# Kernel optimization log

Hardware: AMD Instinct MI355X
Metric: run time of the kernel (lower is better)

Reference implementation:

```python
import jax, jax.numpy as jnp
import numpy as np

N = 20000      # nodes
E = 320000     # edges (before self loops)
IN = 128       # in_channels
HID = 256      # hidden_channels
HEADS = 8
C = HID // HEADS  # 32 per-head dim
L = 4          # num_gat_layers
BN_EPS = 1e-5
LN_EPS = 1e-5


def setup_inputs() -> dict:
    key = jax.random.key(0)
    ks = iter(jax.random.split(key, 64))
    def rn(shape, s=0.05):
        return jax.random.normal(next(ks), shape, jnp.float32) * s
    inp = {
        'x': jax.random.normal(next(ks), (N, IN), jnp.float32),
        'edge_index': jax.random.randint(next(ks), (2, E), 0, N),
        # FeatureMLP
        'mlp_w1': rn((IN, HID)), 'mlp_b1': jnp.zeros((HID,), jnp.float32),
        'bn1_g': jnp.ones((HID,), jnp.float32), 'bn1_b': jnp.zeros((HID,), jnp.float32),
        'mlp_w2': rn((HID, HID)), 'mlp_b2': jnp.zeros((HID,), jnp.float32),
        'bn2_g': jnp.ones((HID,), jnp.float32), 'bn2_b': jnp.zeros((HID,), jnp.float32),
        'mlp_w3': rn((HID, HID)), 'mlp_b3': jnp.zeros((HID,), jnp.float32),
        # stacked GATv2 layer params [L, ...]
        'gat_wl': rn((L, HID, HID)), 'gat_bl': jnp.zeros((L, HID), jnp.float32),
        'gat_wr': rn((L, HID, HID)), 'gat_br': jnp.zeros((L, HID), jnp.float32),
        'gat_att': rn((L, HEADS, C)), 'gat_bias': jnp.zeros((L, HID), jnp.float32),
        'ln_g': jnp.ones((L, HID), jnp.float32), 'ln_b': jnp.zeros((L, HID), jnp.float32),
        'head_w1': rn((2 * HID, HID)), 'head_b1': jnp.zeros((HID,), jnp.float32),
        'hbn1_g': jnp.ones((HID,), jnp.float32), 'hbn1_b': jnp.zeros((HID,), jnp.float32),
        'head_w2': rn((HID, HID // 2)), 'head_b2': jnp.zeros((HID // 2,), jnp.float32),
        'hbn2_g': jnp.ones((HID // 2,), jnp.float32), 'hbn2_b': jnp.zeros((HID // 2,), jnp.float32),
        'head_w3': rn((HID // 2, HID // 4)), 'head_b3': jnp.zeros((HID // 4,), jnp.float32),
        'head_w4': rn((HID // 4, 1)), 'head_b4': jnp.zeros((1,), jnp.float32),
    }
    return inp


def _lrelu01(v):
    return jax.nn.leaky_relu(v, 0.1)


def _bn_eval(v, g, b):
    # eval-mode BatchNorm1d with running_mean=0, running_var=1
    return v * (g / jnp.sqrt(1.0 + BN_EPS)) + b


def _layernorm(v, g, b):
    mu = jnp.mean(v, axis=-1, keepdims=True)
    var = jnp.mean((v - mu) ** 2, axis=-1, keepdims=True)
    return (v - mu) / jnp.sqrt(var + LN_EPS) * g + b


def _gatv2(x, src, dst, Wl, bl, Wr, br, att, bias):
    n = x.shape[0]
    xl = (x @ Wl + bl).reshape(n, HEADS, C)   # source transform
    xr = (x @ Wr + br).reshape(n, HEADS, C)   # target transform
    # per-edge attention logits (GATv2): a . LeakyReLU(x_l[src] + x_r[dst])
    e = jax.nn.leaky_relu(xl[src] + xr[dst], 0.2)          # [E, H, C]
    logits = jnp.einsum('ehc,hc->eh', e, att)               # [E, H]
    # segment softmax over destination nodes
    m = jax.ops.segment_max(logits, dst, num_segments=n)    # [N, H]
    a = jnp.exp(logits - m[dst])
    s = jax.ops.segment_sum(a, dst, num_segments=n)
    alpha = a / (s[dst] + 1e-16)                            # [E, H]
    out = jax.ops.segment_sum(xl[src] * alpha[:, :, None], dst, num_segments=n)
    return out.reshape(n, HID) + bias


def _forward(x, mlp_w1, mlp_b1, bn1_g, bn1_b, mlp_w2, mlp_b2, bn2_g, bn2_b,
             mlp_w3, mlp_b3, gat_wl, gat_bl, gat_wr, gat_br, gat_att, gat_bias,
             ln_g, ln_b, head_w1, head_b1, hbn1_g, hbn1_b, head_w2, head_b2,
             hbn2_g, hbn2_b, head_w3, head_b3, head_w4, head_b4, edge_index):
    n = x.shape[0]
    # FeatureMLP (eval: dropout off)
    h = _lrelu01(_bn_eval(x @ mlp_w1 + mlp_b1, bn1_g, bn1_b))
    h = _lrelu01(_bn_eval(h @ mlp_w2 + mlp_b2, bn2_g, bn2_b))
    x_mlp = h @ mlp_w3 + mlp_b3
    # add self loops
    loop = jnp.arange(n)
    src = jnp.concatenate([edge_index[0], loop])
    dst = jnp.concatenate([edge_index[1], loop])
    g = x_mlp
    for i in range(L):
        res = g
        o = _gatv2(g, src, dst, gat_wl[i], gat_bl[i], gat_wr[i], gat_br[i],
                   gat_att[i], gat_bias[i])
        o = _lrelu01(_layernorm(o, ln_g[i], ln_b[i]))
        g = o + res
    xc = jnp.concatenate([x_mlp, g], axis=1)                # [N, 2*HID]
    h = _lrelu01(_bn_eval(xc @ head_w1 + head_b1, hbn1_g, hbn1_b))
    h = _lrelu01(_bn_eval(h @ head_w2 + head_b2, hbn2_g, hbn2_b))
    h = _lrelu01(h @ head_w3 + head_b3)
    return h @ head_w4 + head_b4                            # [N, 1]


def reference(x, edge_index, mlp_w1, mlp_b1, bn1_g, bn1_b, mlp_w2, mlp_b2,
              bn2_g, bn2_b, mlp_w3, mlp_b3, gat_wl, gat_bl, gat_wr, gat_br,
              gat_att, gat_bias, ln_g, ln_b, head_w1, head_b1, hbn1_g, hbn1_b,
              head_w2, head_b2, hbn2_g, hbn2_b, head_w3, head_b3, head_w4, head_b4):
    return _forward(x, mlp_w1, mlp_b1, bn1_g, bn1_b, mlp_w2, mlp_b2, bn2_g,
                    bn2_b, mlp_w3, mlp_b3, gat_wl, gat_bl, gat_wr, gat_br,
                    gat_att, gat_bias, ln_g, ln_b, head_w1, head_b1, hbn1_g,
                    hbn1_b, head_w2, head_b2, hbn2_g, hbn2_b, head_w3, head_b3,
                    head_w4, head_b4, edge_index)
```

## Files before the change

kernel.cpp:

```cpp
#include <hip/hip_runtime.h>
#include <hip/hip_bf16.h>

#define N_NODES 20000
#define E_EDGES 320000
#define E_TOT   (E_EDGES + N_NODES)
#define IN_CH   128
#define HID     256
#define HEADS   8
#define CPH     32

enum { EP_BIAS = 0, EP_BN_LRELU = 1, EP_LRELU = 2 };

typedef _Float16 f16;
typedef f16  f16x2 __attribute__((ext_vector_type(2)));
typedef f16  f16x4 __attribute__((ext_vector_type(4)));
typedef f16  f16x8 __attribute__((ext_vector_type(8)));
typedef float f32x2 __attribute__((ext_vector_type(2)));
typedef float f32x4 __attribute__((ext_vector_type(4)));

__device__ __forceinline__ f16x2 h2max(f16x2 a, f16x2 b) {
#if __has_builtin(__builtin_elementwise_max)
    return __builtin_elementwise_max(a, b);
#else
    f16x2 r; r[0] = a[0] > b[0] ? a[0] : b[0]; r[1] = a[1] > b[1] ? a[1] : b[1]; return r;
#endif
}
__device__ __forceinline__ float hdot2(f16x2 a, f16x2 b, float c) {
#if __has_builtin(__builtin_amdgcn_fdot2)
    return __builtin_amdgcn_fdot2(a, b, c, false);
#else
    return c + (float)a[0] * (float)b[0] + (float)a[1] * (float)b[1];
#endif
}
__device__ __forceinline__ float fexp2(float x) {
#if __has_builtin(__builtin_amdgcn_exp2f)
    return __builtin_amdgcn_exp2f(x);
#else
    return exp2f(x);
#endif
}

__device__ __forceinline__ size_t frag_idx(int row, int col, int KB) {
    int kb = col >> 6, ks = (col >> 5) & 1, q = (col >> 3) & 3, e = col & 7;
    return ((((size_t)(row >> 4) * KB + kb) * 2 + ks) << 9) + (((q << 4) | (row & 15)) << 3) + e;
}

struct WDesc { const float* src; f16* dst; int K; int Nc; int NTOT; int ct0; };
struct WDescs { WDesc d[14]; };

#define WPREP_BLKS (14 * 512)
#define CVT_BLKS   ((N_NODES * IN_CH) / 256)
#define DEG_BLKS   ((E_EDGES + 255) / 256)
#define ZERO_BLKS  ((N_NODES + 255) / 256)
#define PREP_BLKS  (WPREP_BLKS + CVT_BLKS + DEG_BLKS + ZERO_BLKS)

__global__ __launch_bounds__(256)
void prep_kernel(WDescs ds, const float* __restrict__ x, f16* __restrict__ x16,
                 const int* __restrict__ dstE, int* __restrict__ cnt, int* __restrict__ cur)
{
    const int bx = blockIdx.x;
    const int tid = threadIdx.x;
    if (bx < WPREP_BLKS) {
        WDesc w = ds.d[bx >> 9];
        int i = ((bx & 511) << 8) + tid;
        if (i < w.K * w.Nc) {
            int NT_local = w.Nc >> 4;
            int e  = i & 7;
            int l  = (i >> 3) & 63;
            int r  = i >> 9;
            int ct = r % NT_local;
            int q  = r / NT_local;
            int ks = q & 1;
            int kb = q >> 1;
            int n  = ct * 16 + (l & 15);
            int k  = kb * 64 + ks * 32 + ((l >> 4) << 3) + e;
            size_t di = (((size_t)(kb * 2 + ks) * w.NTOT + w.ct0 + ct) << 9) + (l << 3) + e;
            w.dst[di] = (f16)w.src[(size_t)k * w.Nc + n];
        }
    } else if (bx < WPREP_BLKS + CVT_BLKS) {
        int i = (bx - WPREP_BLKS) * 256 + tid;
        if (i < N_NODES * IN_CH) {
            int row = i / IN_CH, col = i - row * IN_CH;
            x16[frag_idx(row, col, 2)] = (f16)x[i];
        }
    } else if (bx < WPREP_BLKS + CVT_BLKS + DEG_BLKS) {
        int e = (bx - WPREP_BLKS - CVT_BLKS) * 256 + tid;
        if (e < E_EDGES) atomicAdd(&cnt[dstE[e]], 1);
    } else {
        int i = (bx - WPREP_BLKS - CVT_BLKS - DEG_BLKS) * 256 + tid;
        if (i < N_NODES) cur[i] = 0;
    }
}

template<int NT, int NTOT, int WAVES, int RT, int DOT, int OUTF>
__global__ __launch_bounds__(WAVES * 64)
void gemm_kernel(const f16* __restrict__ A1, int KB1,
                 const f16* __restrict__ A2, int KB2,
                 const f16* __restrict__ Wf,
                 const float* __restrict__ biasA,
                 const float* __restrict__ biasB,
                 const float* __restrict__ bng,
                 const float* __restrict__ bnb,
                 f16* __restrict__ out16A,
                 f16* __restrict__ out16B,
                 f16* __restrict__ dup16,
                 float* __restrict__ out32,
                 const float* __restrict__ dotw,
                 const float* __restrict__ dotb,
                 float* __restrict__ outdot,
                 int NcA, int KBo, int mode)
{
    const int tid  = threadIdx.x;
    const int wave = tid >> 6;
    const int lane = tid & 63;
    const int quad = lane >> 4;
    const int rb0 = blockIdx.x * RT;
    const int KBt = KB1 + KB2;

    f32x4 acc[RT][NT];
#pragma unroll
    for (int t = 0; t < RT; ++t)
#pragma unroll
        for (int j = 0; j < NT; ++j) acc[t][j] = (f32x4){0.f, 0.f, 0.f, 0.f};

#pragma unroll 2
    for (int kb = 0; kb < KBt; ++kb) {
#pragma unroll
        for (int ks = 0; ks < 2; ++ks) {
            f16x8 a[RT];
#pragma unroll
            for (int t = 0; t < RT; ++t) {
                const f16* ap = (kb < KB1)
                    ? A1 + (((((size_t)(rb0 + t)) * KB1 + kb) * 2 + ks) << 9) + (lane << 3)
                    : A2 + (((((size_t)(rb0 + t)) * KB2 + (kb - KB1)) * 2 + ks) << 9) + (lane << 3);
                a[t] = *(const f16x8*)ap;
            }
            const f16* bp = Wf + (((size_t)(kb * 2 + ks) * NTOT + wave * NT) << 9) + (lane << 3);
#pragma unroll
            for (int ct = 0; ct < NT; ++ct) {
                f16x8 b = *(const f16x8*)(bp + ((size_t)ct << 9));
#pragma unroll
                for (int t = 0; t < RT; ++t)
                    acc[t][ct] = __builtin_amdgcn_mfma_f32_16x16x32_f16(a[t], b, acc[t][ct], 0, 0, 0);
            }
        }
    }

    const int c0 = lane & 15;
    const int NcB = NTOT * 16 - NcA;
#pragma unroll
    for (int t = 0; t < RT; ++t) {
        const int r0 = (rb0 + t) * 16 + (quad << 2);
#pragma unroll
        for (int ct = 0; ct < NT; ++ct) {
            int col = (wave * NT + ct) * 16 + c0;
            bool isB = col >= NcA;
            int colL = isB ? col - NcA : col;
            float bv = isB ? biasB[colL] : biasA[colL];
            float sc = 1.f, sh = 0.f;
            if (mode == EP_BN_LRELU) {
                sc = bng[col] * rsqrtf(1.f + 1e-5f);
                sh = bnb[col];
            }
#pragma unroll
            for (int reg = 0; reg < 4; ++reg) {
                int row = r0 + reg;
                float v = acc[t][ct][reg] + bv;
                if (mode == EP_BN_LRELU) { v = v * sc + sh; v = v > 0.f ? v : 0.1f * v; }
                else if (mode == EP_LRELU) { v = v > 0.f ? v : 0.1f * v; }
                if (OUTF) {
                    size_t idx = frag_idx(row, col, KBo);
                    out16A[idx] = (f16)v;
                    if (dup16) dup16[idx] = (f16)v;
                    if (out32) out32[(size_t)row * NcA + col] = v;
                } else {
                    f16* Cout = isB ? out16B : out16A;
                    int stride = isB ? NcB : NcA;
                    Cout[(size_t)row * stride + colL] = (f16)v;
                }
            }
        }
    }
}

__global__ __launch_bounds__(512)
void scan_mlp123_kernel(const int* __restrict__ cnt, int* __restrict__ off,
                        const f16* __restrict__ x16,
                        const f16* __restrict__ w1f, const float* __restrict__ b1,
                        const float* __restrict__ bn1g, const float* __restrict__ bn1b,
                        const f16* __restrict__ w2f, const float* __restrict__ b2,
                        const float* __restrict__ bn2g, const float* __restrict__ bn2b,
                        const f16* __restrict__ w3f, const float* __restrict__ b3,
                        f16* __restrict__ x_mlp16, f16* __restrict__ g16, float* __restrict__ g32)
{
    __shared__ f16 hsA[32 * 264];
    __shared__ f16 hsB[32 * 264];
    __shared__ int wsum[8];
    const int tid  = threadIdx.x;
    const int wave = tid >> 6;
    const int lane = tid & 63;

    if (blockIdx.x == 0) {
        int carry = 0;
        for (int r = 0; r < 40; ++r) {
            int i = r * 512 + tid;
            int v = (i < N_NODES) ? cnt[i] + 1 : 0;
            int s = v;
#pragma unroll
            for (int d = 1; d < 64; d <<= 1) { int t = __shfl_up(s, d, 64); if (lane >= d) s += t; }
            if (lane == 63) wsum[wave] = s;
            __syncthreads();
            int woff = 0, tot = 0;
#pragma unroll
            for (int j = 0; j < 8; ++j) { int wj = wsum[j]; tot += wj; if (j < wave) woff += wj; }
            if (i < N_NODES) off[i] = carry + woff + s - v;
            carry += tot;
            __syncthreads();
        }
        if (tid == 0) off[N_NODES] = carry;
        return;
    }

    const int quad = lane >> 4;
    const int c0   = lane & 15;
    const int rb0  = (blockIdx.x - 1) * 2;

    {
        f32x4 acc[2][2];
#pragma unroll
        for (int t = 0; t < 2; ++t)
#pragma unroll
            for (int j = 0; j < 2; ++j) acc[t][j] = (f32x4){0.f, 0.f, 0.f, 0.f};
#pragma unroll
        for (int kb = 0; kb < 2; ++kb) {
#pragma unroll
            for (int ks = 0; ks < 2; ++ks) {
                f16x8 a[2];
#pragma unroll
                for (int t = 0; t < 2; ++t)
                    a[t] = *(const f16x8*)(x16 + (((((size_t)(rb0 + t)) * 2 + kb) * 2 + ks) << 9) + (lane << 3));
                const f16* bp = w1f + (((size_t)(kb * 2 + ks) * 16 + wave * 2) << 9) + (lane << 3);
#pragma unroll
                for (int ct = 0; ct < 2; ++ct) {
                    f16x8 b = *(const f16x8*)(bp + ((size_t)ct << 9));
#pragma unroll
                    for (int t = 0; t < 2; ++t)
                        acc[t][ct] = __builtin_amdgcn_mfma_f32_16x16x32_f16(a[t], b, acc[t][ct], 0, 0, 0);
                }
            }
        }
#pragma unroll
        for (int t = 0; t < 2; ++t) {
            const int r0 = t * 16 + (quad << 2);
#pragma unroll
            for (int ct = 0; ct < 2; ++ct) {
                const int col = (wave * 2 + ct) * 16 + c0;
                const float sc = bn1g[col] * rsqrtf(1.f + 1e-5f);
                const float sh = bn1b[col];
                const float bv = b1[col];
#pragma unroll
                for (int reg = 0; reg < 4; ++reg) {
                    float v = acc[t][ct][reg] + bv;
                    v = v * sc + sh;
                    v = v > 0.f ? v : 0.1f * v;
                    hsA[(r0 + reg) * 264 + col] = (f16)v;
                }
            }
        }
    }
    __syncthreads();

    {
        f32x4 acc[2][2];
#pragma unroll
        for (int t = 0; t < 2; ++t)
#pragma unroll
            for (int j = 0; j < 2; ++j) acc[t][j] = (f32x4){0.f, 0.f, 0.f, 0.f};
#pragma unroll
        for (int kb = 0; kb < 4; ++kb) {
#pragma unroll
            for (int ks = 0; ks < 2; ++ks) {
                const int kofs = kb * 64 + ks * 32 + ((lane >> 4) << 3);
                f16x8 a[2];
#pragma unroll
                for (int t = 0; t < 2; ++t)
                    a[t] = *(const f16x8*)&hsA[(t * 16 + (lane & 15)) * 264 + kofs];
                const f16* bp = w2f + (((size_t)(kb * 2 + ks) * 16 + wave * 2) << 9) + (lane << 3);
#pragma unroll
                for (int ct = 0; ct < 2; ++ct) {
                    f16x8 b = *(const f16x8*)(bp + ((size_t)ct << 9));
#pragma unroll
                    for (int t = 0; t < 2; ++t)
                        acc[t][ct] = __builtin_amdgcn_mfma_f32_16x16x32_f16(a[t], b, acc[t][ct], 0, 0, 0);
                }
            }
        }
#pragma unroll
        for (int t = 0; t < 2; ++t) {
            const int r0 = t * 16 + (quad << 2);
#pragma unroll
            for (int ct = 0; ct < 2; ++ct) {
                const int col = (wave * 2 + ct) * 16 + c0;
                const float sc = bn2g[col] * rsqrtf(1.f + 1e-5f);
                const float sh = bn2b[col];
                const float bv = b2[col];
#pragma unroll
                for (int reg = 0; reg < 4; ++reg) {
                    float v = acc[t][ct][reg] + bv;
                    v = v * sc + sh;
                    v = v > 0.f ? v : 0.1f * v;
                    hsB[(r0 + reg) * 264 + col] = (f16)v;
                }
            }
        }
    }
    __syncthreads();

    {
        f32x4 acc[2][2];
#pragma unroll
        for (int t = 0; t < 2; ++t)
#pragma unroll
            for (int j = 0; j < 2; ++j) acc[t][j] = (f32x4){0.f, 0.f, 0.f, 0.f};
#pragma unroll
        for (int kb = 0; kb < 4; ++kb) {
#pragma unroll
            for (int ks = 0; ks < 2; ++ks) {
                const int kofs = kb * 64 + ks * 32 + ((lane >> 4) << 3);
                f16x8 a[2];
#pragma unroll
                for (int t = 0; t < 2; ++t)
                    a[t] = *(const f16x8*)&hsB[(t * 16 + (lane & 15)) * 264 + kofs];
                const f16* bp = w3f + (((size_t)(kb * 2 + ks) * 16 + wave * 2) << 9) + (lane << 3);
#pragma unroll
                for (int ct = 0; ct < 2; ++ct) {
                    f16x8 b = *(const f16x8*)(bp + ((size_t)ct << 9));
#pragma unroll
                    for (int t = 0; t < 2; ++t)
                        acc[t][ct] = __builtin_amdgcn_mfma_f32_16x16x32_f16(a[t], b, acc[t][ct], 0, 0, 0);
                }
            }
        }
#pragma unroll
        for (int t = 0; t < 2; ++t) {
#pragma unroll
            for (int ct = 0; ct < 2; ++ct) {
                const int col = (wave * 2 + ct) * 16 + c0;
                const float bv = b3[col];
#pragma unroll
                for (int reg = 0; reg < 4; ++reg) {
                    const int row = (rb0 + t) * 16 + (quad << 2) + reg;
                    float v = acc[t][ct][reg] + bv;
                    size_t idx = frag_idx(row, col, 4);
                    x_mlp16[idx] = (f16)v;
                    g16[idx] = (f16)v;
                    g32[(size_t)row * HID + col] = v;
                }
            }
        }
    }
}

#define FILL_BLKS ((E_TOT + 511) / 512)

__global__ __launch_bounds__(512)
void fill_gemm0_kernel(const int* __restrict__ src, const int* __restrict__ dst,
                       const int* __restrict__ off, int* __restrict__ cur, int* __restrict__ csr,
                       const f16* __restrict__ g16, const f16* __restrict__ w0f,
                       const float* __restrict__ bl, const float* __restrict__ br,
                       f16* __restrict__ xl, f16* __restrict__ xr)
{
    const int tid = threadIdx.x;
    if (blockIdx.x < FILL_BLKS) {
        int i = blockIdx.x * 512 + tid;
        if (i < E_EDGES) {
            int d = dst[i];
            int pos = atomicAdd(&cur[d], 1);
            csr[off[d] + pos] = src[i];
        } else if (i < E_TOT) {
            int j = i - E_EDGES;
            csr[off[j + 1] - 1] = j;
        }
        return;
    }

    const int wave = tid >> 6;
    const int lane = tid & 63;
    const int quad = lane >> 4;
    const int c0   = lane & 15;
    const int rb0  = (blockIdx.x - FILL_BLKS) * 2;
    f32x4 acc[2][4];
#pragma unroll
    for (int t = 0; t < 2; ++t)
#pragma unroll
        for (int j = 0; j < 4; ++j) acc[t][j] = (f32x4){0.f, 0.f, 0.f, 0.f};
#pragma unroll 2
    for (int kb = 0; kb < 4; ++kb) {
#pragma unroll
        for (int ks = 0; ks < 2; ++ks) {
            f16x8 a[2];
#pragma unroll
            for (int t = 0; t < 2; ++t)
                a[t] = *(const f16x8*)(g16 + (((((size_t)(rb0 + t)) * 4 + kb) * 2 + ks) << 9) + (lane << 3));
            const f16* bp = w0f + (((size_t)(kb * 2 + ks) * 32 + wave * 4) << 9) + (lane << 3);
#pragma unroll
            for (int ct = 0; ct < 4; ++ct) {
                f16x8 b = *(const f16x8*)(bp + ((size_t)ct << 9));
#pragma unroll
                for (int t = 0; t < 2; ++t)
                    acc[t][ct] = __builtin_amdgcn_mfma_f32_16x16x32_f16(a[t], b, acc[t][ct], 0, 0, 0);
            }
        }
    }
#pragma unroll
    for (int t = 0; t < 2; ++t) {
        const int r0 = (rb0 + t) * 16 + (quad << 2);
#pragma unroll
        for (int ct = 0; ct < 4; ++ct) {
            const int col = (wave * 4 + ct) * 16 + c0;
            const bool isR = col >= HID;
            const int colL = col & (HID - 1);
            const float bv = isR ? br[colL] : bl[colL];
            f16* Cout = isR ? xr : xl;
#pragma unroll
            for (int reg = 0; reg < 4; ++reg)
                Cout[(size_t)(r0 + reg) * HID + colL] = (f16)(acc[t][ct][reg] + bv);
        }
    }
}

__global__ __launch_bounds__(512)
void head123_kernel(const f16* __restrict__ xm,
                    const f16* __restrict__ g16,
                    const f16* __restrict__ w1f,
                    const float* __restrict__ b1,
                    const float* __restrict__ bn1g, const float* __restrict__ bn1b,
                    const f16* __restrict__ w2f,
                    const float* __restrict__ b2,
                    const float* __restrict__ bn2g, const float* __restrict__ bn2b,
                    const f16* __restrict__ w3f,
                    const float* __restrict__ b3,
                    const float* __restrict__ w4, const float* __restrict__ b4,
                    float* __restrict__ out)
{
    __shared__ f16  hsA[32 * 264];
    __shared__ f16  hsB[32 * 136];
    __shared__ float red[32][65];
    const int tid  = threadIdx.x;
    const int wave = tid >> 6;
    const int lane = tid & 63;
    const int quad = lane >> 4;
    const int c0   = lane & 15;
    const int rb0  = blockIdx.x * 2;

    {
        f32x4 acc[2][2];
#pragma unroll
        for (int t = 0; t < 2; ++t)
#pragma unroll
            for (int j = 0; j < 2; ++j) acc[t][j] = (f32x4){0.f, 0.f, 0.f, 0.f};
#pragma unroll 2
        for (int kb = 0; kb < 8; ++kb) {
#pragma unroll
            for (int ks = 0; ks < 2; ++ks) {
                f16x8 a[2];
#pragma unroll
                for (int t = 0; t < 2; ++t) {
                    const f16* ap = (kb < 4)
                        ? xm  + (((((size_t)(rb0 + t)) * 4 + kb) * 2 + ks) << 9) + (lane << 3)
                        : g16 + (((((size_t)(rb0 + t)) * 4 + (kb - 4)) * 2 + ks) << 9) + (lane << 3);
                    a[t] = *(const f16x8*)ap;
                }
                const f16* bp = w1f + (((size_t)(kb * 2 + ks) * 16 + wave * 2) << 9) + (lane << 3);
#pragma unroll
                for (int ct = 0; ct < 2; ++ct) {
                    f16x8 b = *(const f16x8*)(bp + ((size_t)ct << 9));
#pragma unroll
                    for (int t = 0; t < 2; ++t)
                        acc[t][ct] = __builtin_amdgcn_mfma_f32_16x16x32_f16(a[t], b, acc[t][ct], 0, 0, 0);
                }
            }
        }
#pragma unroll
        for (int t = 0; t < 2; ++t) {
            const int r0 = t * 16 + (quad << 2);
#pragma unroll
            for (int ct = 0; ct < 2; ++ct) {
                const int col = (wave * 2 + ct) * 16 + c0;
                const float sc = bn1g[col] * rsqrtf(1.f + 1e-5f);
                const float sh = bn1b[col];
                const float bv = b1[col];
#pragma unroll
                for (int reg = 0; reg < 4; ++reg) {
                    float v = acc[t][ct][reg] + bv;
                    v = v * sc + sh;
                    v = v > 0.f ? v : 0.1f * v;
                    hsA[(r0 + reg) * 264 + col] = (f16)v;
                }
            }
        }
    }
    __syncthreads();

    {
        f32x4 acc[2];
        acc[0] = (f32x4){0.f, 0.f, 0.f, 0.f};
        acc[1] = (f32x4){0.f, 0.f, 0.f, 0.f};
#pragma unroll
        for (int kb = 0; kb < 4; ++kb) {
#pragma unroll
            for (int ks = 0; ks < 2; ++ks) {
                const int kofs = kb * 64 + ks * 32 + ((lane >> 4) << 3);
                f16x8 a0 = *(const f16x8*)&hsA[(lane & 15) * 264 + kofs];
                f16x8 a1 = *(const f16x8*)&hsA[(16 + (lane & 15)) * 264 + kofs];
                f16x8 b  = *(const f16x8*)(w2f + (((size_t)(kb * 2 + ks) * 8 + wave) << 9) + (lane << 3));
                acc[0] = __builtin_amdgcn_mfma_f32_16x16x32_f16(a0, b, acc[0], 0, 0, 0);
                acc[1] = __builtin_amdgcn_mfma_f32_16x16x32_f16(a1, b, acc[1], 0, 0, 0);
            }
        }
        const int col = wave * 16 + c0;
        const float sc = bn2g[col] * rsqrtf(1.f + 1e-5f);
        const float sh = bn2b[col];
        const float bv = b2[col];
#pragma unroll
        for (int t = 0; t < 2; ++t) {
            const int r0 = t * 16 + (quad << 2);
#pragma unroll
            for (int reg = 0; reg < 4; ++reg) {
                float v = acc[t][reg] + bv;
                v = v * sc + sh;
                v = v > 0.f ? v : 0.1f * v;
                hsB[(r0 + reg) * 136 + col] = (f16)v;
            }
        }
    }
    __syncthreads();

    {
        const int rbL = wave >> 2;
        const int ct3 = wave & 3;
        f32x4 acc = (f32x4){0.f, 0.f, 0.f, 0.f};
#pragma unroll
        for (int ksl = 0; ksl < 4; ++ksl) {
            const int arow = rbL * 16 + (lane & 15);
            f16x8 a = *(const f16x8*)&hsB[arow * 136 + ksl * 32 + ((lane >> 4) << 3)];
            f16x8 b = *(const f16x8*)(w3f + (((size_t)(ksl * 4 + ct3)) << 9) + (lane << 3));
            acc = __builtin_amdgcn_mfma_f32_16x16x32_f16(a, b, acc, 0, 0, 0);
        }
        const int col = ct3 * 16 + c0;
        const float wv = w4[col];
        const float bv = b3[col];
        const int r0 = rbL * 16 + (quad << 2);
#pragma unroll
        for (int reg = 0; reg < 4; ++reg) {
            float v = acc[reg] + bv;
            v = v > 0.f ? v : 0.1f * v;
            red[r0 + reg][col] = v * wv;
        }
    }
    __syncthreads();

    {
        const int row = wave * 4 + (lane >> 4);
        float pr = red[row][c0] + red[row][c0 + 16] + red[row][c0 + 32] + red[row][c0 + 48];
        pr += __shfl_xor(pr, 1, 64);
        pr += __shfl_xor(pr, 2, 64);
        pr += __shfl_xor(pr, 4, 64);
        pr += __shfl_xor(pr, 8, 64);
        if (c0 == 0) out[blockIdx.x * 32 + row] = pr + b4[0];
    }
}

__global__ __launch_bounds__(256)
void gat_agg_kernel(const f16* __restrict__ xl, const f16* __restrict__ xr,
                    float* __restrict__ g, f16* __restrict__ g16,
                    const int* __restrict__ off, const int* __restrict__ csr,
                    const float* __restrict__ att,
                    const float* __restrict__ bias,
                    const float* __restrict__ lng,
                    const float* __restrict__ lnb)
{
    const int wv   = threadIdx.x >> 6;
    const int ln   = threadIdx.x & 63;
    const int half = ln >> 5;
    const int lp   = ln & 31;
    const int n    = blockIdx.x * 4 + wv;
    if (n >= N_NODES) return;

    const f16x8* xl8 = (const f16x8*)xl;
    f16x8 xrv = ((const f16x8*)xr)[n * 32 + lp];
    f16x2 xr0; xr0[0] = xrv[0]; xr0[1] = xrv[1];
    f16x2 xr1; xr1[0] = xrv[2]; xr1[1] = xrv[3];
    f16x2 xr2; xr2[0] = xrv[4]; xr2[1] = xrv[5];
    f16x2 xr3; xr3[0] = xrv[6]; xr3[1] = xrv[7];
    float4 af0 = ((const float4*)att)[lp * 2];
    float4 af1 = ((const float4*)att)[lp * 2 + 1];
    const float L2E = 1.44269504f;
    f16x2 av0; av0[0] = (f16)(af0.x * L2E); av0[1] = (f16)(af0.y * L2E);
    f16x2 av1; av1[0] = (f16)(af0.z * L2E); av1[1] = (f16)(af0.w * L2E);
    f16x2 av2; av2[0] = (f16)(af1.x * L2E); av2[1] = (f16)(af1.y * L2E);
    f16x2 av3; av3[0] = (f16)(af1.z * L2E); av3[1] = (f16)(af1.w * L2E);
    const f16x2 k02 = { (f16)0.2f, (f16)0.2f };

    float s = 0.f;
    float o0 = 0.f, o1 = 0.f, o2 = 0.f, o3 = 0.f, o4 = 0.f, o5 = 0.f, o6 = 0.f, o7 = 0.f;

    int p = off[n], end = off[n + 1];

    auto procv = [&](f16x8 xv, bool valid) {
        f16x2 x0; x0[0] = xv[0]; x0[1] = xv[1];
        f16x2 x1; x1[0] = xv[2]; x1[1] = xv[3];
        f16x2 x2; x2[0] = xv[4]; x2[1] = xv[5];
        f16x2 x3; x3[0] = xv[6]; x3[1] = xv[7];
        f16x2 v0 = x0 + xr0, v1 = x1 + xr1, v2 = x2 + xr2, v3 = x3 + xr3;
        v0 = h2max(v0, v0 * k02); v1 = h2max(v1, v1 * k02);
        v2 = h2max(v2, v2 * k02); v3 = h2max(v3, v3 * k02);
        float pr = hdot2(v0, av0, hdot2(v1, av1, hdot2(v2, av2, hdot2(v3, av3, 0.f))));
        pr += __shfl_xor(pr, 1, 64);
        pr += __shfl_xor(pr, 2, 64);
        float e = valid ? fexp2(pr) : 0.f;
        s += e;
        o0 = fmaf((float)xv[0], e, o0); o1 = fmaf((float)xv[1], e, o1);
        o2 = fmaf((float)xv[2], e, o2); o3 = fmaf((float)xv[3], e, o3);
        o4 = fmaf((float)xv[4], e, o4); o5 = fmaf((float)xv[5], e, o5);
        o6 = fmaf((float)xv[6], e, o6); o7 = fmaf((float)xv[7], e, o7);
    };
    auto proc = [&](int ep) {
        bool valid = ep < end;
        int sidx = csr[valid ? ep : end - 1];
        procv(xl8[(size_t)sidx * 32 + lp], valid);
    };

    for (; p + 16 <= end; p += 16) {
        int sA = csr[p +      half];
        int sB = csr[p + 2  + half];
        int sC = csr[p + 4  + half];
        int sD = csr[p + 6  + half];
        int sE = csr[p + 8  + half];
        int sF = csr[p + 10 + half];
        int sG = csr[p + 12 + half];
        int sH = csr[p + 14 + half];
        f16x8 rA = xl8[(size_t)sA * 32 + lp];
        f16x8 rB = xl8[(size_t)sB * 32 + lp];
        f16x8 rC = xl8[(size_t)sC * 32 + lp];
        f16x8 rD = xl8[(size_t)sD * 32 + lp];
        f16x8 rE = xl8[(size_t)sE * 32 + lp];
        f16x8 rF = xl8[(size_t)sF * 32 + lp];
        f16x8 rG = xl8[(size_t)sG * 32 + lp];
        f16x8 rH = xl8[(size_t)sH * 32 + lp];
        procv(rA, true); procv(rB, true); procv(rC, true); procv(rD, true);
        procv(rE, true); procv(rF, true); procv(rG, true); procv(rH, true);
    }
    for (; p + 8 <= end; p += 8) {
        int sA = csr[p +     half];
        int sB = csr[p + 2 + half];
        int sC = csr[p + 4 + half];
        int sD = csr[p + 6 + half];
        f16x8 rA = xl8[(size_t)sA * 32 + lp];
        f16x8 rB = xl8[(size_t)sB * 32 + lp];
        f16x8 rC = xl8[(size_t)sC * 32 + lp];
        f16x8 rD = xl8[(size_t)sD * 32 + lp];
        procv(rA, true); procv(rB, true); procv(rC, true); procv(rD, true);
    }
    for (; p + 4 <= end; p += 4) {
        int sA = csr[p +     half];
        int sB = csr[p + 2 + half];
        f16x8 rA = xl8[(size_t)sA * 32 + lp];
        f16x8 rB = xl8[(size_t)sB * 32 + lp];
        procv(rA, true); procv(rB, true);
    }
    for (; p < end; p += 2) proc(p + half);

    s  += __shfl_xor(s, 32, 64);
    o0 += __shfl_xor(o0, 32, 64); o1 += __shfl_xor(o1, 32, 64);
    o2 += __shfl_xor(o2, 32, 64); o3 += __shfl_xor(o3, 32, 64);
    o4 += __shfl_xor(o4, 32, 64); o5 += __shfl_xor(o5, 32, 64);
    o6 += __shfl_xor(o6, 32, 64); o7 += __shfl_xor(o7, 32, 64);

    const int lidx = lp * 2 + half;
    float q0 = half ? o4 : o0;
    float q1 = half ? o5 : o1;
    float q2 = half ? o6 : o2;
    float q3 = half ? o7 : o3;

    float inv = 1.f / (s + 1e-16f);
    float4 bi = ((const float4*)bias)[lidx];
    float y0 = q0 * inv + bi.x;
    float y1 = q1 * inv + bi.y;
    float y2 = q2 * inv + bi.z;
    float y3 = q3 * inv + bi.w;

    float s1 = y0 + y1 + y2 + y3;
    float s2 = y0 * y0 + y1 * y1 + y2 * y2 + y3 * y3;
#pragma unroll
    for (int d = 32; d; d >>= 1) { s1 += __shfl_xor(s1, d, 64); s2 += __shfl_xor(s2, d, 64); }
    float mu  = s1 * (1.f / HID);
    float ex2 = s2 * (1.f / HID);
    float rstd = rsqrtf(ex2 - mu * mu + 1e-5f);
    float4 lg = ((const float4*)lng)[lidx];
    float4 lb = ((const float4*)lnb)[lidx];
    float nv0 = (y0 - mu) * rstd * lg.x + lb.x; nv0 = nv0 > 0.f ? nv0 : 0.1f * nv0;
    float nv1 = (y1 - mu) * rstd * lg.y + lb.y; nv1 = nv1 > 0.f ? nv1 : 0.1f * nv1;
    float nv2 = (y2 - mu) * rstd * lg.z + lb.z; nv2 = nv2 > 0.f ? nv2 : 0.1f * nv2;
    float nv3 = (y3 - mu) * rstd * lg.w + lb.w; nv3 = nv3 > 0.f ? nv3 : 0.1f * nv3;

    float4 gv = ((const float4*)g)[n * 64 + lidx];
    float g0 = nv0 + gv.x, g1 = nv1 + gv.y, g2 = nv2 + gv.z, g3 = nv3 + gv.w;
    ((float4*)g)[n * 64 + lidx] = make_float4(g0, g1, g2, g3);
    f16x4 gh; gh[0] = (f16)g0; gh[1] = (f16)g1; gh[2] = (f16)g2; gh[3] = (f16)g3;
    *(f16x4*)&g16[frag_idx(n, 4 * lidx, 4)] = gh;
}

static inline size_t align_up(size_t v, size_t a) { return (v + a - 1) & ~(a - 1); }

extern "C" void kernel_launch(void* const* d_in, const int* in_sizes, int n_in,
                              void* d_out, int out_size, void* d_ws, size_t ws_size,
                              hipStream_t stream)
{
    const float* x      = (const float*)d_in[0];
    const int*   ei     = (const int*)d_in[1];
    const float* mlp_w1 = (const float*)d_in[2];
    const float* mlp_b1 = (const float*)d_in[3];
    const float* bn1_g  = (const float*)d_in[4];
    const float* bn1_b  = (const float*)d_in[5];
    const float* mlp_w2 = (const float*)d_in[6];
    const float* mlp_b2 = (const float*)d_in[7];
    const float* bn2_g  = (const float*)d_in[8];
    const float* bn2_b  = (const float*)d_in[9];
    const float* mlp_w3 = (const float*)d_in[10];
    const float* mlp_b3 = (const float*)d_in[11];
    const float* gat_wl = (const float*)d_in[12];
    const float* gat_bl = (const float*)d_in[13];
    const float* gat_wr = (const float*)d_in[14];
    const float* gat_br = (const float*)d_in[15];
    const float* gat_att  = (const float*)d_in[16];
    const float* gat_bias = (const float*)d_in[17];
    const float* ln_g   = (const float*)d_in[18];
    const float* ln_b   = (const float*)d_in[19];
    const float* head_w1 = (const float*)d_in[20];
    const float* head_b1 = (const float*)d_in[21];
    const float* hbn1_g  = (const float*)d_in[22];
    const float* hbn1_b  = (const float*)d_in[23];
    const float* head_w2 = (const float*)d_in[24];
    const float* head_b2 = (const float*)d_in[25];
    const float* hbn2_g  = (const float*)d_in[26];
    const float* hbn2_b  = (const float*)d_in[27];
    const float* head_w3 = (const float*)d_in[28];
    const float* head_b3 = (const float*)d_in[29];
    const float* head_w4 = (const float*)d_in[30];
    const float* head_b4 = (const float*)d_in[31];
    float* out = (float*)d_out;

    char* w = (char*)d_ws;
    size_t p = 0;
    int* off  = (int*)(w + p); p = align_up(p + (N_NODES + 1) * sizeof(int), 64);
    int* fill = (int*)(w + p); p = align_up(p + N_NODES * sizeof(int), 64);
    int* cur  = (int*)(w + p); p = align_up(p + N_NODES * sizeof(int), 64);
    int* csr  = (int*)(w + p); p = align_up(p + E_TOT * sizeof(int), 64);
    float* g32 = (float*)(w + p); p = align_up(p + (size_t)N_NODES * HID * 4, 64);
    auto halloc = [&](size_t elems) {
        f16* q = (f16*)(w + p);
        p = align_up(p + elems * 2, 1024);
        return q;
    };
    f16* x16     = halloc((size_t)N_NODES * IN_CH);
    f16* x_mlp16 = halloc((size_t)N_NODES * HID);
    f16* g16     = halloc((size_t)N_NODES * HID);
    f16* xl16    = halloc((size_t)N_NODES * HID);
    f16* xr16    = halloc((size_t)N_NODES * HID);
    f16* wt_mlp1 = halloc((size_t)IN_CH * HID);
    f16* wt_mlp2 = halloc((size_t)HID * HID);
    f16* wt_mlp3 = halloc((size_t)HID * HID);
    f16* wt_g[4];
    for (int i = 0; i < 4; ++i) wt_g[i] = halloc((size_t)HID * 2 * HID);
    f16* wt_h1 = halloc((size_t)2 * HID * HID);
    f16* wt_h2 = halloc((size_t)HID * (HID / 2));
    f16* wt_h3 = halloc((size_t)(HID / 2) * (HID / 4));
    (void)ws_size; (void)in_sizes; (void)n_in; (void)out_size;

    const int* e_src = ei;
    const int* e_dst = ei + E_EDGES;

    dim3 blk(256);
    dim3 gM625((N_NODES + 31) / 32);

    WDescs ds;
    ds.d[0]  = { mlp_w1, wt_mlp1, IN_CH, HID, 16, 0 };
    ds.d[1]  = { mlp_w2, wt_mlp2, HID, HID, 16, 0 };
    ds.d[2]  = { mlp_w3, wt_mlp3, HID, HID, 16, 0 };
    for (int i = 0; i < 4; ++i) {
        ds.d[3 + 2 * i] = { gat_wl + (size_t)i * HID * HID, wt_g[i], HID, HID, 32, 0 };
        ds.d[4 + 2 * i] = { gat_wr + (size_t)i * HID * HID, wt_g[i], HID, HID, 32, 16 };
    }
    ds.d[11] = { head_w1, wt_h1, 2 * HID, HID, 16, 0 };
    ds.d[12] = { head_w2, wt_h2, HID, HID / 2, 8, 0 };
    ds.d[13] = { head_w3, wt_h3, HID / 2, HID / 4, 4, 0 };

    hipMemsetAsync(fill, 0, N_NODES * sizeof(int), stream);
    prep_kernel<<<dim3(PREP_BLKS), blk, 0, stream>>>(ds, x, x16, e_dst, fill, cur);

    scan_mlp123_kernel<<<dim3(1 + 625), dim3(512), 0, stream>>>(fill, off, x16,
        wt_mlp1, mlp_b1, bn1_g, bn1_b,
        wt_mlp2, mlp_b2, bn2_g, bn2_b,
        wt_mlp3, mlp_b3, x_mlp16, g16, g32);
    fill_gemm0_kernel<<<dim3(FILL_BLKS + 625), dim3(512), 0, stream>>>(e_src, e_dst, off, cur, csr,
        g16, wt_g[0], gat_bl, gat_br, xl16, xr16);

    gat_agg_kernel<<<(N_NODES + 3) / 4, blk, 0, stream>>>(xl16, xr16, g32, g16, off, csr,
                                                          gat_att, gat_bias, ln_g, ln_b);
    for (int i = 1; i < 4; ++i) {
        gemm_kernel<4, 32, 8, 2, 0, 0><<<gM625, 512, 0, stream>>>(g16, 4, nullptr, 0, wt_g[i],
            gat_bl + i * HID, gat_br + i * HID, nullptr, nullptr,
            xl16, xr16, nullptr, nullptr, nullptr, nullptr, nullptr, HID, 0, EP_BIAS);
        gat_agg_kernel<<<(N_NODES + 3) / 4, blk, 0, stream>>>(xl16, xr16, g32, g16, off, csr,
                                                              gat_att + i * HID, gat_bias + i * HID,
                                                              ln_g + i * HID, ln_b + i * HID);
    }

    head123_kernel<<<gM625, dim3(512), 0, stream>>>(x_mlp16, g16,
        wt_h1, head_b1, hbn1_g, hbn1_b,
        wt_h2, head_b2, hbn2_g, hbn2_b,
        wt_h3, head_b3, head_w4, head_b4, out);
}
```

Before: 405.4 us.

## Split each node's edge list across two waves in GAT aggregation

The aggregation kernel now uses 512 threads per block with two waves per destination node. Each wave handles half of the node's incoming edges, and the partial softmax sums and weighted accumulators are combined through shared memory before the layernorm epilogue. This doubles the number of wavefronts gathering neighbour features, to hide gather latency and shorten per-node serial loops. The cost is a block-wide barrier, extra shared-memory traffic, and half the waves sitting idle during the epilogue.

```diff
diff --git a/kernel.cpp b/kernel.cpp
--- a/kernel.cpp
+++ b/kernel.cpp
@@ -571,7 +571,7 @@
     }
 }
 
-__global__ __launch_bounds__(256)
+__global__ __launch_bounds__(512)
 void gat_agg_kernel(const f16* __restrict__ xl, const f16* __restrict__ xr,
                     float* __restrict__ g, f16* __restrict__ g16,
                     const int* __restrict__ off, const int* __restrict__ csr,
@@ -580,12 +580,15 @@
                     const float* __restrict__ lng,
                     const float* __restrict__ lnb)
 {
-    const int wv   = threadIdx.x >> 6;
-    const int ln   = threadIdx.x & 63;
+    __shared__ float comb[4][9][65];
+    const int tid  = threadIdx.x;
+    const int wv8  = tid >> 6;
+    const int ni   = wv8 >> 1;
+    const int sub  = wv8 & 1;
+    const int ln   = tid & 63;
     const int half = ln >> 5;
     const int lp   = ln & 31;
-    const int n    = blockIdx.x * 4 + wv;
-    if (n >= N_NODES) return;
+    const int n    = blockIdx.x * 4 + ni;
 
     const f16x8* xl8 = (const f16x8*)xl;
     f16x8 xrv = ((const f16x8*)xr)[n * 32 + lp];
@@ -605,7 +608,10 @@
     float s = 0.f;
     float o0 = 0.f, o1 = 0.f, o2 = 0.f, o3 = 0.f, o4 = 0.f, o5 = 0.f, o6 = 0.f, o7 = 0.f;
 
-    int p = off[n], end = off[n + 1];
+    const int p0 = off[n], end0 = off[n + 1];
+    const int h1 = (end0 - p0 + 1) >> 1;
+    int p   = sub ? p0 + h1 : p0;
+    const int end = sub ? end0 : p0 + h1;
 
     auto procv = [&](f16x8 xv, bool valid) {
         f16x2 x0; x0[0] = xv[0]; x0[1] = xv[1];
@@ -627,7 +633,7 @@
     };
     auto proc = [&](int ep) {
         bool valid = ep < end;
-        int sidx = csr[valid ? ep : end - 1];
+        int sidx = csr[valid ? ep : p0];
         procv(xl8[(size_t)sidx * 32 + lp], valid);
     };
 
@@ -676,6 +682,17 @@
     o2 += __shfl_xor(o2, 32, 64); o3 += __shfl_xor(o3, 32, 64);
     o4 += __shfl_xor(o4, 32, 64); o5 += __shfl_xor(o5, 32, 64);
     o6 += __shfl_xor(o6, 32, 64); o7 += __shfl_xor(o7, 32, 64);
+
+    if (sub) {
+        comb[ni][0][ln] = s;
+        comb[ni][1][ln] = o0; comb[ni][2][ln] = o1; comb[ni][3][ln] = o2; comb[ni][4][ln] = o3;
+        comb[ni][5][ln] = o4; comb[ni][6][ln] = o5; comb[ni][7][ln] = o6; comb[ni][8][ln] = o7;
+    }
+    __syncthreads();
+    if (sub) return;
+    s  += comb[ni][0][ln];
+    o0 += comb[ni][1][ln]; o1 += comb[ni][2][ln]; o2 += comb[ni][3][ln]; o3 += comb[ni][4][ln];
+    o4 += comb[ni][5][ln]; o5 += comb[ni][6][ln]; o6 += comb[ni][7][ln]; o7 += comb[ni][8][ln];
 
     const int lidx = lp * 2 + half;
     float q0 = half ? o4 : o0;
@@ -806,15 +823,15 @@
     fill_gemm0_kernel<<<dim3(FILL_BLKS + 625), dim3(512), 0, stream>>>(e_src, e_dst, off, cur, csr,
         g16, wt_g[0], gat_bl, gat_br, xl16, xr16);
 
-    gat_agg_kernel<<<(N_NODES + 3) / 4, blk, 0, stream>>>(xl16, xr16, g32, g16, off, csr,
-                                                          gat_att, gat_bias, ln_g, ln_b);
+    gat_agg_kernel<<<dim3(N_NODES / 4), dim3(512), 0, stream>>>(xl16, xr16, g32, g16, off, csr,
+                                                                gat_att, gat_bias, ln_g, ln_b);
     for (int i = 1; i < 4; ++i) {
         gemm_kernel<4, 32, 8, 2, 0, 0><<<gM625, 512, 0, stream>>>(g16, 4, nullptr, 0, wt_g[i],
             gat_bl + i * HID, gat_br + i * HID, nullptr, nullptr,
             xl16, xr16, nullptr, nullptr, nullptr, nullptr, nullptr, HID, 0, EP_BIAS);
-        gat_agg_kernel<<<(N_NODES + 3) / 4, blk, 0, stream>>>(xl16, xr16, g32, g16, off, csr,
-                                                              gat_att + i * HID, gat_bias + i * HID,
-                                                              ln_g + i * HID, ln_b + i * HID);
+        gat_agg_kernel<<<dim3(N_NODES / 4), dim3(512), 0, stream>>>(xl16, xr16, g32, g16, off, csr,
+                                                                    gat_att + i * HID, gat_bias + i * HID,
+                                                                    ln_g + i * HID, ln_b + i * HID);
     }
 
     head123_kernel<<<gM625, dim3(512), 0, stream>>>(x_mlp16, g16,
```

After: 462.6 us. 14.1% more time.
